# Performance work log

Measured on AMD Instinct MI355X. Metric: run time of the kernel, lower is better.

## Reference

```python
import jax, jax.numpy as jnp
import numpy as np

# ---- model dims (match init_kwargs) ----
B, L, D_MODEL = 2, 4096, 1024
EXPAND = 2
D_INNER = EXPAND * D_MODEL          # 2048
D_STATE = 128
D_CONV = 4
HEADDIM = 64
NHEADS = D_INNER // HEADDIM         # 32
NGROUPS = 1
CHUNK = 256
CONV_DIM = D_INNER + 2 * NGROUPS * D_STATE   # 2304
D_IN = 2 * D_INNER + 2 * NGROUPS * D_STATE + NHEADS  # 4384
EPS = 1e-5
DT_MIN, DT_MAX, DT_FLOOR = 0.001, 0.1, 1e-4
DT_LIMIT = (0.0, 100.0)
CONV_INIT = 0.5


def setup_inputs() -> dict:
    key = jax.random.key(0)
    ks = jax.random.split(key, 6)
    zxbcdt = jax.random.normal(ks[0], (B, L, D_IN), jnp.float32)
    conv_weight = jax.random.uniform(ks[1], (CONV_DIM, D_CONV), jnp.float32, -CONV_INIT, CONV_INIT)
    conv_b = jax.random.normal(ks[2], (CONV_DIM,), jnp.float32) * 0.01
    # dt_bias init: inverse softplus of dt sampled log-uniform in [dt_min, dt_max]
    dt = jnp.exp(jax.random.uniform(ks[3], (NHEADS,), jnp.float32) * (np.log(DT_MAX) - np.log(DT_MIN)) + np.log(DT_MIN))
    dt = jnp.clip(dt, DT_FLOOR, None)
    dt_bias = dt + jnp.log(-jnp.expm1(-dt))
    A_log = jnp.log(jax.random.uniform(ks[4], (NHEADS,), jnp.float32, 1.0, 16.0))
    Dparam = jnp.ones((NHEADS,), jnp.float32)
    norm_weight = jnp.ones((D_INNER,), jnp.float32)
    return dict(zxbcdt=zxbcdt, conv_weight=conv_weight, conv_b=conv_b,
                dt_bias=dt_bias, A_log=A_log, Dparam=Dparam, norm_weight=norm_weight)


def _segsum(x):
    """x: (..., T) -> (..., T, T), entry [i,j] = sum_{j<k<=i} x[k], -inf above diag."""
    T = x.shape[-1]
    xc = jnp.cumsum(x, axis=-1)
    seg = xc[..., :, None] - xc[..., None, :]
    mask = jnp.tril(jnp.ones((T, T), dtype=bool))
    return jnp.where(mask, seg, -jnp.inf)


def _ssd(x, a, Bm, Cm, chunk):
    """Chunked SSD (Mamba2). x:(b,l,h,p) already dt-scaled, a:(b,l,h)=dt*A,
    Bm/Cm:(b,l,h,n). Returns y:(b,l,h,p)."""
    b, l, h, p = x.shape
    n = Bm.shape[-1]
    c = l // chunk
    x = x.reshape(b, c, chunk, h, p)
    Bm = Bm.reshape(b, c, chunk, h, n)
    Cm = Cm.reshape(b, c, chunk, h, n)
    a = a.reshape(b, c, chunk, h).transpose(0, 3, 1, 2)  # (b,h,c,cl)
    a_cs = jnp.cumsum(a, axis=-1)                        # (b,h,c,cl)
    # 1) intra-chunk (diagonal blocks)
    Lmat = jnp.exp(_segsum(a))                           # (b,h,c,cl,cl)
    Y_diag = jnp.einsum('bclhn,bcshn,bhcls,bcshp->bclhp', Cm, Bm, Lmat, x)
    # 2) chunk final states
    decay_states = jnp.exp(a_cs[..., -1:] - a_cs)        # (b,h,c,cl)
    states = jnp.einsum('bclhn,bhcl,bclhp->bchpn', Bm, decay_states, x)
    states = jnp.concatenate([jnp.zeros_like(states[:, :1]), states], axis=1)  # (b,c+1,h,p,n)
    # 3) inter-chunk recurrence
    chunk_sum = jnp.pad(a_cs[..., -1], ((0, 0), (0, 0), (1, 0)))  # (b,h,c+1)
    decay_chunk = jnp.exp(_segsum(chunk_sum))            # (b,h,c+1,c+1)
    new_states = jnp.einsum('bhzc,bchpn->bzhpn', decay_chunk, states)
    prev_states = new_states[:, :-1]                     # (b,c,h,p,n)
    # 4) state -> output contribution
    Y_off = jnp.einsum('bclhn,bchpn,bhcl->bclhp', Cm, prev_states, jnp.exp(a_cs))
    return (Y_diag + Y_off).reshape(b, l, h, p)


def reference(zxbcdt, conv_weight, conv_b, dt_bias, A_log, Dparam, norm_weight):
    z, xBC, dt_raw = jnp.split(zxbcdt, [D_INNER, D_INNER + CONV_DIM], axis=-1)
    # depthwise causal conv1d (padding=d_conv-1, truncate to L) + SiLU
    xp = jnp.pad(xBC, ((0, 0), (D_CONV - 1, 0), (0, 0)))
    conv = conv_b
    for k in range(D_CONV):  # small fixed kernel width
        conv = conv + conv_weight[:, k] * xp[:, k:k + L, :]
    xBC = jax.nn.silu(conv)
    x, Bm, Cm = jnp.split(xBC, [D_INNER, D_INNER + NGROUPS * D_STATE], axis=-1)
    x = x.reshape(B, L, NHEADS, HEADDIM)
    hpg = NHEADS // NGROUPS
    Bm = jnp.repeat(Bm.reshape(B, L, NGROUPS, D_STATE), hpg, axis=2)  # (B,L,H,N)
    Cm = jnp.repeat(Cm.reshape(B, L, NGROUPS, D_STATE), hpg, axis=2)
    dt = jax.nn.softplus(dt_raw + dt_bias)               # (B,L,H)
    dt = jnp.clip(dt, DT_LIMIT[0], DT_LIMIT[1])
    A = -jnp.exp(A_log)                                  # (H,)
    y = _ssd(x * dt[..., None], dt * A, Bm, Cm, CHUNK)   # (B,L,H,P)
    y = y + x * Dparam[None, None, :, None]              # skip term D*x
    y = y.reshape(B, L, D_INNER)
    # gated RMSNorm (norm_before_gate=False): normalize(y * silu(z)) * w
    y = y * jax.nn.silu(z)
    y = y * jax.lax.rsqrt(jnp.mean(y * y, axis=-1, keepdims=True) + EPS) * norm_weight
    return y
```

## Files before the change

### kernel.cpp

```cpp
#include <hip/hip_runtime.h>
#include <hip/hip_bf16.h>

#define NB 2
#define LSEQ 4096
#define DIN 4384
#define DINNER 2048
#define DSTATE 128
#define CONVD 2304
#define HD 64
#define NH 32
#define CK 256
#define NCH 16

typedef __attribute__((ext_vector_type(8))) short bfrag;
typedef __attribute__((ext_vector_type(4))) float ffrag;

__device__ __forceinline__ float bf2f(unsigned short u){ return __uint_as_float(((unsigned int)u)<<16); }
__device__ __forceinline__ unsigned short f2bf(float f){
  unsigned int u = __float_as_uint(f);
  unsigned int r = (u + 0x7fffu + ((u>>16)&1u)) >> 16;
  return (unsigned short)r;
}
__device__ __forceinline__ unsigned int pk2(float a, float b){
  return (unsigned)f2bf(a) | ((unsigned)f2bf(b) << 16);
}
__device__ __forceinline__ float blo(unsigned int u){ return __uint_as_float(u<<16); }
__device__ __forceinline__ float bhi(unsigned int u){ return __uint_as_float(u & 0xffff0000u); }
__device__ __forceinline__ bfrag pack8(const float* f){
  bfrag r;
  #pragma unroll
  for (int i=0;i<8;i++) r[i] = (short)f2bf(f[i]);
  return r;
}

__global__ __launch_bounds__(256) void k_conv(const float* __restrict__ zx,
    const float* __restrict__ cw, const float* __restrict__ cb,
    unsigned short* __restrict__ xconv)
{
  int bid = blockIdx.x;
  int ct = bid % 9;
  int rt = bid / 9;
  int b = rt >> 6, lt = rt & 63;
  int t = threadIdx.x;
  int q = t & 63, lg = t >> 6;
  int c0 = ct*256 + q*4;
  const float* colp = zx + (size_t)b*LSEQ*DIN + DINNER + c0;
  float4 w0 = *(const float4*)&cw[(c0+0)*4];
  float4 w1 = *(const float4*)&cw[(c0+1)*4];
  float4 w2 = *(const float4*)&cw[(c0+2)*4];
  float4 w3 = *(const float4*)&cw[(c0+3)*4];
  float4 bias = *(const float4*)&cb[c0];
  int l0 = lt*64 + lg*16;
  float4 win0, win1, win2, win3;
  win0 = (l0-3 >= 0) ? *(const float4*)(colp + (size_t)(l0-3)*DIN) : make_float4(0,0,0,0);
  win1 = (l0-2 >= 0) ? *(const float4*)(colp + (size_t)(l0-2)*DIN) : make_float4(0,0,0,0);
  win2 = (l0-1 >= 0) ? *(const float4*)(colp + (size_t)(l0-1)*DIN) : make_float4(0,0,0,0);
  unsigned short* op = xconv + (size_t)(b*LSEQ)*CONVD + c0;
  #pragma unroll 4
  for (int i=0;i<16;i++){
    int l = l0 + i;
    win3 = *(const float4*)(colp + (size_t)l*DIN);
    float o0 = bias.x + w0.x*win0.x + w0.y*win1.x + w0.z*win2.x + w0.w*win3.x;
    float o1 = bias.y + w1.x*win0.y + w1.y*win1.y + w1.z*win2.y + w1.w*win3.y;
    float o2 = bias.z + w2.x*win0.z + w2.y*win1.z + w2.z*win2.z + w2.w*win3.z;
    float o3 = bias.w + w3.x*win0.w + w3.y*win1.w + w3.z*win2.w + w3.w*win3.w;
    o0 = o0 / (1.f + __expf(-o0));
    o1 = o1 / (1.f + __expf(-o1));
    o2 = o2 / (1.f + __expf(-o2));
    o3 = o3 / (1.f + __expf(-o3));
    uint2 pk; pk.x = pk2(o0,o1); pk.y = pk2(o2,o3);
    *(uint2*)&op[(size_t)l*CONVD] = pk;
    win0 = win1; win1 = win2; win2 = win3;
  }
}

__global__ __launch_bounds__(256) void k_dt(const float* __restrict__ zx,
    const float* __restrict__ dtb, float* __restrict__ dtv)
{
  int idx = blockIdx.x*256 + threadIdx.x;
  int l = idx & (LSEQ-1);
  int bh = idx >> 12;
  int h = bh & 31, b = bh >> 5;
  float x = zx[(size_t)(b*LSEQ + l)*DIN + DINNER + CONVD + h] + dtb[h];
  float sp = (x > 20.f) ? x : log1pf(__expf(x));
  dtv[idx] = fminf(sp, 100.f);
}

__global__ __launch_bounds__(256) void k_tr(const unsigned short* __restrict__ xconv,
    unsigned short* __restrict__ btg)
{
  __shared__ unsigned short sT[128][72];
  int bid = blockIdx.x;
  int b = bid >> 6, tile = bid & 63;
  int l0 = tile * 64;
  int t = threadIdx.x;
  #pragma unroll
  for (int k=0;k<32;k++){
    int idx = 256*k + t;
    int l = idx >> 7, n = idx & 127;
    sT[n][l] = xconv[(size_t)(b*LSEQ + l0 + l)*CONVD + DINNER + n];
  }
  __syncthreads();
  #pragma unroll
  for (int k=0;k<32;k++){
    int idx = 256*k + t;
    int n = idx >> 6, l = idx & 63;
    btg[(size_t)(b*DSTATE + n)*LSEQ + l0 + l] = sT[n][l];
  }
}

__constant__ int g_lt[10] = {0,1,1,2,2,2,3,3,3,3};
__constant__ int g_st[10] = {0,0,1,0,1,2,0,1,2,3};
__global__ __launch_bounds__(256) void k_gmat(const unsigned short* __restrict__ xconv,
    unsigned short* __restrict__ G)
{
  int bid = blockIdx.x;
  int pr = bid % 10;
  int cc = bid / 10;
  int c = cc & 15, b = cc >> 4;
  int lt = g_lt[pr], st = g_st[pr];
  int t = threadIdx.x, lane = t & 63, wv = t >> 6;
  int cq = lane & 15, g = lane >> 4;
  const unsigned short* base = xconv + (size_t)(b*LSEQ + c*CK)*CONVD;
  ffrag acc[4];
  #pragma unroll
  for (int ss=0; ss<4; ++ss){ acc[ss][0]=0.f; acc[ss][1]=0.f; acc[ss][2]=0.f; acc[ss][3]=0.f; }
  #pragma unroll
  for (int ks=0; ks<4; ++ks){
    int nb = 32*ks + 8*g;
    int l = lt*64 + 16*wv + cq;
    bfrag afr = *(const bfrag*)(base + (size_t)l*CONVD + DINNER + DSTATE + nb);
    #pragma unroll
    for (int ss=0; ss<4; ++ss){
      int s = st*64 + 16*ss + cq;
      bfrag bfr = *(const bfrag*)(base + (size_t)s*CONVD + DINNER + nb);
      acc[ss] = __builtin_amdgcn_mfma_f32_16x16x32_bf16(afr, bfr, acc[ss], 0,0,0);
    }
  }
  unsigned short* gp = G + (size_t)(b*NCH + c)*CK*CK;
  #pragma unroll
  for (int ss=0; ss<4; ++ss)
    #pragma unroll
    for (int j=0; j<4; ++j){
      int l = lt*64 + 16*wv + 4*g + j, s = st*64 + 16*ss + cq;
      gp[(size_t)l*CK + s] = f2bf(acc[ss][j]);
    }
}

__global__ __launch_bounds__(256) void k_states(const unsigned short* __restrict__ xconv,
   const unsigned short* __restrict__ btg,
   const float* __restrict__ dtv, const float* __restrict__ alog,
   unsigned short* __restrict__ states,
   float* __restrict__ acsg2)
{
  int bid = blockIdx.x;
  int h = bid & 31, c = (bid>>5)&15, b = bid>>9;
  int t = threadIdx.x, lane = t & 63, wv = t >> 6;
  int cq = lane & 15, g = lane >> 4;
  __shared__ float s_acs2[CK];
  __shared__ float s_w[CK];
  __shared__ float s_dt[CK];
  __shared__ unsigned short s_xsT[64][256];

  const float LOG2E = 1.44269504088896340736f;
  float dtl = dtv[(size_t)(b*NH + h)*LSEQ + c*CK + t];
  float a2 = dtl * (-__expf(alog[h])) * LOG2E;
  s_dt[t] = dtl;
  s_acs2[t] = a2;
  __syncthreads();
  #pragma unroll
  for (int off=1; off<256; off<<=1){
    float v = (t>=off) ? s_acs2[t-off] : 0.f;
    __syncthreads();
    s_acs2[t] += v;
    __syncthreads();
  }
  float a2last = s_acs2[CK-1];
  s_w[t] = exp2f(a2last - s_acs2[t]);
  acsg2[((size_t)(b*NCH + c)*NH + h)*CK + t] = s_acs2[t];
  {
    const unsigned short* xp = xconv + (size_t)(b*LSEQ + c*CK)*CONVD + h*HD;
    int p = t & 63;
    int lw = t >> 6;
    #pragma unroll 8
    for (int k=0;k<64;k++){
      int l = 4*k + lw;
      float x = bf2f(xp[(size_t)l*CONVD + p]);
      s_xsT[p][l ^ ((p&7)<<3)] = f2bf(x * s_dt[l]);
    }
  }
  __syncthreads();

  ffrag acc[4][2];
  #pragma unroll
  for (int ps=0;ps<4;ps++)
    #pragma unroll
    for (int ns=0;ns<2;ns++){ acc[ps][ns][0]=0.f; acc[ps][ns][1]=0.f; acc[ps][ns][2]=0.f; acc[ps][ns][3]=0.f; }
  const unsigned short* btp = btg + (size_t)b*DSTATE*LSEQ + c*CK;
  #pragma unroll 2
  for (int ks=0; ks<8; ++ks){
    int lb = 32*ks + 8*g;
    float4 w0 = *(const float4*)&s_w[lb];
    float4 w1 = *(const float4*)&s_w[lb+4];
    bfrag bfr[2];
    #pragma unroll
    for (int ns=0; ns<2; ++ns){
      int n = 32*wv + 16*ns + cq;
      bfr[ns] = *(const bfrag*)(btp + (size_t)n*LSEQ + lb);
    }
    bfrag afr[4];
    #pragma unroll
    for (int ps=0; ps<4; ++ps){
      int p = 16*ps + cq;
      bfrag xv = *(const bfrag*)&s_xsT[p][lb ^ ((p&7)<<3)];
      float f[8];
      f[0]=bf2f((unsigned short)xv[0])*w0.x; f[1]=bf2f((unsigned short)xv[1])*w0.y;
      f[2]=bf2f((unsigned short)xv[2])*w0.z; f[3]=bf2f((unsigned short)xv[3])*w0.w;
      f[4]=bf2f((unsigned short)xv[4])*w1.x; f[5]=bf2f((unsigned short)xv[5])*w1.y;
      f[6]=bf2f((unsigned short)xv[6])*w1.z; f[7]=bf2f((unsigned short)xv[7])*w1.w;
      afr[ps] = pack8(f);
    }
    #pragma unroll
    for (int ps=0; ps<4; ++ps)
      #pragma unroll
      for (int ns=0; ns<2; ++ns)
        acc[ps][ns] = __builtin_amdgcn_mfma_f32_16x16x32_bf16(afr[ps], bfr[ns], acc[ps][ns], 0,0,0);
  }
  size_t sbase = ((size_t)((b*NCH + c)*NH + h))*HD*DSTATE;
  #pragma unroll
  for (int ps=0; ps<4; ++ps)
    #pragma unroll
    for (int ns=0; ns<2; ++ns)
      #pragma unroll
      for (int j=0; j<4; ++j){
        int p = 16*ps + 4*g + j, n = 32*wv + 16*ns + cq;
        states[sbase + (size_t)p*DSTATE + n] = f2bf(acc[ps][ns][j]);
      }
}

__global__ __launch_bounds__(256) void k_scan(unsigned short* __restrict__ states,
    const float* __restrict__ acsg2)
{
  int bid = blockIdx.x;
  int sub = bid & 7, h = (bid>>3) & 31, b = bid >> 8;
  int t = threadIdx.x;
  int e0 = sub*1024 + t*4;
  float c0=0.f, c1=0.f, c2=0.f, c3=0.f;
  for (int c=0;c<NCH;c++){
    float dec = exp2f(acsg2[((size_t)(b*NCH + c)*NH + h)*CK + (CK-1)]);
    size_t base = ((size_t)((b*NCH + c)*NH + h))*HD*DSTATE + e0;
    uint2 v = *(uint2*)&states[base];
    float u0 = blo(v.x), u1 = bhi(v.x), u2 = blo(v.y), u3 = bhi(v.y);
    uint2 w; w.x = pk2(c0,c1); w.y = pk2(c2,c3);
    *(uint2*)&states[base] = w;
    c0 = dec*c0 + u0; c1 = dec*c1 + u1; c2 = dec*c2 + u2; c3 = dec*c3 + u3;
  }
}

__global__ __launch_bounds__(256) void k_Y(const unsigned short* __restrict__ xconv,
   const float* __restrict__ dtv,
   const unsigned short* __restrict__ G,
   const unsigned short* __restrict__ states,
   const float* __restrict__ acsg2,
   unsigned short* __restrict__ ybuf)
{
  int bid = blockIdx.x;
  int h = bid & 31, c = (bid>>5)&15, b = bid>>9;
  int t = threadIdx.x, lane = t & 63, wv = t >> 6;
  int cq = lane & 15, g = lane >> 4;
  __shared__ float s_acs2[CK];
  __shared__ float s_dt[CK];
  __shared__ unsigned short s_xsT[64][256];

  s_acs2[t] = acsg2[((size_t)(b*NCH + c)*NH + h)*CK + t];
  s_dt[t] = dtv[(size_t)(b*NH + h)*LSEQ + c*CK + t];
  __syncthreads();
  {
    const unsigned short* xp = xconv + (size_t)(b*LSEQ + c*CK)*CONVD + h*HD;
    int p = t & 63;
    int lw = t >> 6;
    #pragma unroll 8
    for (int k=0;k<64;k++){
      int l = 4*k + lw;
      float x = bf2f(xp[(size_t)l*CONVD + p]);
      s_xsT[p][l ^ ((p&7)<<3)] = f2bf(x * s_dt[l]);
    }
  }
  __syncthreads();

  ffrag acc[4][4];
  #pragma unroll
  for (int ls=0;ls<4;ls++)
    #pragma unroll
    for (int ps=0;ps<4;ps++){ acc[ls][ps][0]=0.f; acc[ls][ps][1]=0.f; acc[ls][ps][2]=0.f; acc[ls][ps][3]=0.f; }
  float a2l[4];
  #pragma unroll
  for (int ls=0; ls<4; ++ls) a2l[ls] = s_acs2[64*wv + 16*ls + cq];

  const unsigned short* gp = G + (size_t)(b*NCH + c)*CK*CK;
  int nks = 2*wv + 2;
  for (int ks=0; ks<nks; ++ks){
    int sb = 32*ks + 8*g;
    float4 e0 = *(const float4*)&s_acs2[sb];
    float4 e1 = *(const float4*)&s_acs2[sb+4];
    float a2s[8] = {e0.x,e0.y,e0.z,e0.w,e1.x,e1.y,e1.z,e1.w};
    bfrag bfr[4];
    #pragma unroll
    for (int ps=0; ps<4; ++ps){
      int p = 16*ps + cq;
      bfr[ps] = *(const bfrag*)&s_xsT[p][sb ^ ((p&7)<<3)];
    }
    bfrag afr[4];
    #pragma unroll
    for (int ls=0; ls<4; ++ls){
      int l = 64*wv + 16*ls + cq;
      bfrag gv = *(const bfrag*)(gp + (size_t)l*CK + sb);
      float f[8];
      #pragma unroll
      for (int i=0;i<8;i++){
        int s = sb + i;
        float cf = exp2f(a2l[ls] - a2s[i]);
        cf = (s <= l) ? cf : 0.f;
        f[i] = bf2f((unsigned short)gv[i]) * cf;
      }
      afr[ls] = pack8(f);
    }
    #pragma unroll
    for (int ls=0; ls<4; ++ls)
      #pragma unroll
      for (int ps=0; ps<4; ++ps)
        acc[ls][ps] = __builtin_amdgcn_mfma_f32_16x16x32_bf16(afr[ls], bfr[ps], acc[ls][ps], 0,0,0);
  }

  {
    float el[4];
    #pragma unroll
    for (int ls=0; ls<4; ++ls) el[ls] = exp2f(a2l[ls]);
    const unsigned short* crow = xconv + (size_t)(b*LSEQ + c*CK)*CONVD + DINNER + DSTATE;
    const unsigned short* psb = states + ((size_t)((b*NCH + c)*NH + h))*HD*DSTATE;
    #pragma unroll
    for (int ks=0; ks<4; ++ks){
      int nb = 32*ks + 8*g;
      bfrag bfr[4];
      #pragma unroll
      for (int pp=0; pp<4; ++pp)
        bfr[pp] = *(const bfrag*)(psb + (size_t)(16*pp + cq)*DSTATE + nb);
      bfrag afr[4];
      #pragma unroll
      for (int ls=0; ls<4; ++ls){
        int l = 64*wv + 16*ls + cq;
        bfrag cv = *(const bfrag*)(crow + (size_t)l*CONVD + nb);
        float f[8];
        #pragma unroll
        for (int i=0;i<8;i++) f[i] = bf2f((unsigned short)cv[i]) * el[ls];
        afr[ls] = pack8(f);
      }
      #pragma unroll
      for (int ls=0; ls<4; ++ls)
        #pragma unroll
        for (int pp=0; pp<4; ++pp)
          acc[ls][pp] = __builtin_amdgcn_mfma_f32_16x16x32_bf16(afr[ls], bfr[pp], acc[ls][pp], 0,0,0);
    }
  }

  unsigned short* yrow = ybuf + (size_t)(b*LSEQ + c*CK)*DINNER + h*HD;
  #pragma unroll
  for (int ls=0; ls<4; ++ls)
    #pragma unroll
    for (int ps=0; ps<4; ++ps)
      #pragma unroll
      for (int j=0; j<4; ++j){
        int l = 64*wv + 16*ls + 4*g + j, p = 16*ps + cq;
        yrow[(size_t)l*DINNER + p] = f2bf(acc[ls][ps][j]);
      }
}

__global__ __launch_bounds__(256) void k_final(const float* __restrict__ zx,
  const unsigned short* __restrict__ xconv, const unsigned short* __restrict__ ybuf,
  const float* __restrict__ dpar, const float* __restrict__ nw,
  float* __restrict__ out)
{
  int row = blockIdx.x;
  int t = threadIdx.x;
  int d0 = 8*t;
  const float* zrow = zx + (size_t)row*DIN;
  const unsigned short* xrow = xconv + (size_t)row*CONVD;
  const unsigned short* yrow = ybuf + (size_t)row*DINNER;
  float vals[8];
  float ss = 0.f;
  uint4 yv = *(const uint4*)&yrow[d0];
  uint4 xv = *(const uint4*)&xrow[d0];
  float4 z0 = *(const float4*)&zrow[d0];
  float4 z1 = *(const float4*)&zrow[d0+4];
  float dp = dpar[d0 >> 6];
  float yf[8], xf[8];
  yf[0]=blo(yv.x); yf[1]=bhi(yv.x); yf[2]=blo(yv.y); yf[3]=bhi(yv.y);
  yf[4]=blo(yv.z); yf[5]=bhi(yv.z); yf[6]=blo(yv.w); yf[7]=bhi(yv.w);
  xf[0]=blo(xv.x); xf[1]=bhi(xv.x); xf[2]=blo(xv.y); xf[3]=bhi(xv.y);
  xf[4]=blo(xv.z); xf[5]=bhi(xv.z); xf[6]=blo(xv.w); xf[7]=bhi(xv.w);
  float zf[8] = {z0.x,z0.y,z0.z,z0.w,z1.x,z1.y,z1.z,z1.w};
  #pragma unroll
  for (int e=0;e<8;e++){
    float y = yf[e] + xf[e]*dp;
    float z = zf[e];
    y *= z / (1.f + __expf(-z));
    vals[e] = y;
    ss += y*y;
  }
  #pragma unroll
  for (int off=1; off<64; off<<=1) ss += __shfl_xor(ss, off, 64);
  __shared__ float red[4];
  if ((t & 63) == 0) red[t>>6] = ss;
  __syncthreads();
  float tot = red[0]+red[1]+red[2]+red[3];
  float rms = rsqrtf(tot * (1.f/(float)DINNER) + 1e-5f);
  float* orow = out + (size_t)row*DINNER;
  float4 w0 = *(const float4*)&nw[d0];
  float4 w1 = *(const float4*)&nw[d0+4];
  float4 o0, o1;
  o0.x = vals[0]*rms*w0.x; o0.y = vals[1]*rms*w0.y;
  o0.z = vals[2]*rms*w0.z; o0.w = vals[3]*rms*w0.w;
  o1.x = vals[4]*rms*w1.x; o1.y = vals[5]*rms*w1.y;
  o1.z = vals[6]*rms*w1.z; o1.w = vals[7]*rms*w1.w;
  *(float4*)&orow[d0] = o0;
  *(float4*)&orow[d0+4] = o1;
}

extern "C" void kernel_launch(void* const* d_in, const int* in_sizes, int n_in,
                              void* d_out, int out_size, void* d_ws, size_t ws_size,
                              hipStream_t stream)
{
  const float* zx   = (const float*)d_in[0];
  const float* cw   = (const float*)d_in[1];
  const float* cb   = (const float*)d_in[2];
  const float* dtb  = (const float*)d_in[3];
  const float* alog = (const float*)d_in[4];
  const float* dpar = (const float*)d_in[5];
  const float* nw   = (const float*)d_in[6];
  float* out = (float*)d_out;
  char* ws = (char*)d_ws;

  unsigned short* xconv  = (unsigned short*)(ws);
  unsigned short* btg    = (unsigned short*)(ws + 37748736);
  float*          dtv    = (float*)(ws + 39845888);
  float*          acsg2  = (float*)(ws + 40894464);
  unsigned short* states = (unsigned short*)(ws + 41943040);
  unsigned short* G      = (unsigned short*)(ws + 58720256);
  unsigned short* ybuf   = (unsigned short*)(ws + 62914560);

  hipLaunchKernelGGL(k_conv,   dim3(NB*64*9), dim3(256), 0, stream, zx, cw, cb, xconv);
  hipLaunchKernelGGL(k_dt,     dim3(1024),  dim3(256), 0, stream, zx, dtb, dtv);
  hipLaunchKernelGGL(k_tr,     dim3(NB*64), dim3(256), 0, stream, xconv, btg);
  hipLaunchKernelGGL(k_gmat,   dim3(NB*NCH*10), dim3(256), 0, stream, xconv, G);
  hipLaunchKernelGGL(k_states, dim3(NB*NCH*NH), dim3(256), 0, stream, xconv, btg, dtv, alog, states, acsg2);
  hipLaunchKernelGGL(k_scan,   dim3(NB*NH*8),  dim3(256), 0, stream, states, acsg2);
  hipLaunchKernelGGL(k_Y,      dim3(NB*NCH*NH), dim3(256), 0, stream, xconv, dtv, G, states, acsg2, ybuf);
  hipLaunchKernelGGL(k_final,  dim3(NB*LSEQ), dim3(256), 0, stream, zx, xconv, ybuf, dpar, nw, out);
}
```

Measured before the change: 342.9 us.

## Merge small kernels, use hardware bf16 pack, wave-shuffle scan, precompute weights

Merges the dt, B-transpose and G-matrix kernels into one launch, split by block-index ranges. Replaces software bf16 rounding with the v_cvt_pk_bf16_f32 instruction and the shared-memory scan in k_states with a wave shuffle scan. It also folds the decay weight into the staged x tile so the MFMA loop needs no per-element rescaling. In k_Y, the inter-chunk C·state term now runs first with a post-scale by exp(acs), and intra-chunk decay factors come from a running product instead of one exp2 per element, which changes rounding slightly.

```diff
diff --git a/kernel.cpp b/kernel.cpp
--- a/kernel.cpp
+++ b/kernel.cpp
@@ -26,11 +26,16 @@
 }
 __device__ __forceinline__ float blo(unsigned int u){ return __uint_as_float(u<<16); }
 __device__ __forceinline__ float bhi(unsigned int u){ return __uint_as_float(u & 0xffff0000u); }
-__device__ __forceinline__ bfrag pack8(const float* f){
-  bfrag r;
-  #pragma unroll
-  for (int i=0;i<8;i++) r[i] = (short)f2bf(f[i]);
+__device__ __forceinline__ unsigned int cvtpk(float a, float b){
+  unsigned int r;
+  asm("v_cvt_pk_bf16_f32 %0, %1, %2" : "=v"(r) : "v"(a), "v"(b));
   return r;
+}
+__device__ __forceinline__ bfrag pack8c(const float* f){
+  union { unsigned int u[4]; bfrag b; } r;
+  r.u[0]=cvtpk(f[0],f[1]); r.u[1]=cvtpk(f[2],f[3]);
+  r.u[2]=cvtpk(f[4],f[5]); r.u[3]=cvtpk(f[6],f[7]);
+  return r.b;
 }
 
 __global__ __launch_bounds__(256) void k_conv(const float* __restrict__ zx,
@@ -68,83 +73,80 @@
     o1 = o1 / (1.f + __expf(-o1));
     o2 = o2 / (1.f + __expf(-o2));
     o3 = o3 / (1.f + __expf(-o3));
-    uint2 pk; pk.x = pk2(o0,o1); pk.y = pk2(o2,o3);
+    uint2 pk; pk.x = cvtpk(o0,o1); pk.y = cvtpk(o2,o3);
     *(uint2*)&op[(size_t)l*CONVD] = pk;
     win0 = win1; win1 = win2; win2 = win3;
   }
 }
 
-__global__ __launch_bounds__(256) void k_dt(const float* __restrict__ zx,
-    const float* __restrict__ dtb, float* __restrict__ dtv)
-{
-  int idx = blockIdx.x*256 + threadIdx.x;
-  int l = idx & (LSEQ-1);
-  int bh = idx >> 12;
-  int h = bh & 31, b = bh >> 5;
-  float x = zx[(size_t)(b*LSEQ + l)*DIN + DINNER + CONVD + h] + dtb[h];
-  float sp = (x > 20.f) ? x : log1pf(__expf(x));
-  dtv[idx] = fminf(sp, 100.f);
-}
-
-__global__ __launch_bounds__(256) void k_tr(const unsigned short* __restrict__ xconv,
-    unsigned short* __restrict__ btg)
+__constant__ int g_lt[10] = {0,1,1,2,2,2,3,3,3,3};
+__constant__ int g_st[10] = {0,0,1,0,1,2,0,1,2,3};
+__global__ __launch_bounds__(256) void k_misc(const float* __restrict__ zx,
+    const float* __restrict__ dtb,
+    const unsigned short* __restrict__ xconv,
+    float* __restrict__ dtv, unsigned short* __restrict__ btg,
+    unsigned short* __restrict__ G)
 {
   __shared__ unsigned short sT[128][72];
   int bid = blockIdx.x;
-  int b = bid >> 6, tile = bid & 63;
-  int l0 = tile * 64;
   int t = threadIdx.x;
-  #pragma unroll
-  for (int k=0;k<32;k++){
-    int idx = 256*k + t;
-    int l = idx >> 7, n = idx & 127;
-    sT[n][l] = xconv[(size_t)(b*LSEQ + l0 + l)*CONVD + DINNER + n];
-  }
-  __syncthreads();
-  #pragma unroll
-  for (int k=0;k<32;k++){
-    int idx = 256*k + t;
-    int n = idx >> 6, l = idx & 63;
-    btg[(size_t)(b*DSTATE + n)*LSEQ + l0 + l] = sT[n][l];
-  }
-}
-
-__constant__ int g_lt[10] = {0,1,1,2,2,2,3,3,3,3};
-__constant__ int g_st[10] = {0,0,1,0,1,2,0,1,2,3};
-__global__ __launch_bounds__(256) void k_gmat(const unsigned short* __restrict__ xconv,
-    unsigned short* __restrict__ G)
-{
-  int bid = blockIdx.x;
-  int pr = bid % 10;
-  int cc = bid / 10;
-  int c = cc & 15, b = cc >> 4;
-  int lt = g_lt[pr], st = g_st[pr];
-  int t = threadIdx.x, lane = t & 63, wv = t >> 6;
-  int cq = lane & 15, g = lane >> 4;
-  const unsigned short* base = xconv + (size_t)(b*LSEQ + c*CK)*CONVD;
-  ffrag acc[4];
-  #pragma unroll
-  for (int ss=0; ss<4; ++ss){ acc[ss][0]=0.f; acc[ss][1]=0.f; acc[ss][2]=0.f; acc[ss][3]=0.f; }
-  #pragma unroll
-  for (int ks=0; ks<4; ++ks){
-    int nb = 32*ks + 8*g;
-    int l = lt*64 + 16*wv + cq;
-    bfrag afr = *(const bfrag*)(base + (size_t)l*CONVD + DINNER + DSTATE + nb);
-    #pragma unroll
-    for (int ss=0; ss<4; ++ss){
-      int s = st*64 + 16*ss + cq;
-      bfrag bfr = *(const bfrag*)(base + (size_t)s*CONVD + DINNER + nb);
-      acc[ss] = __builtin_amdgcn_mfma_f32_16x16x32_bf16(afr, bfr, acc[ss], 0,0,0);
-    }
-  }
-  unsigned short* gp = G + (size_t)(b*NCH + c)*CK*CK;
-  #pragma unroll
-  for (int ss=0; ss<4; ++ss)
-    #pragma unroll
-    for (int j=0; j<4; ++j){
-      int l = lt*64 + 16*wv + 4*g + j, s = st*64 + 16*ss + cq;
-      gp[(size_t)l*CK + s] = f2bf(acc[ss][j]);
-    }
+  if (bid < 320){
+    int pr = bid % 10;
+    int cc = bid / 10;
+    int c = cc & 15, b = cc >> 4;
+    int lt = g_lt[pr], st = g_st[pr];
+    int lane = t & 63, wv = t >> 6;
+    int cq = lane & 15, g = lane >> 4;
+    const unsigned short* base = xconv + (size_t)(b*LSEQ + c*CK)*CONVD;
+    ffrag acc[4];
+    #pragma unroll
+    for (int ss=0; ss<4; ++ss){ acc[ss][0]=0.f; acc[ss][1]=0.f; acc[ss][2]=0.f; acc[ss][3]=0.f; }
+    #pragma unroll
+    for (int ks=0; ks<4; ++ks){
+      int nb = 32*ks + 8*g;
+      int l = lt*64 + 16*wv + cq;
+      bfrag afr = *(const bfrag*)(base + (size_t)l*CONVD + DINNER + DSTATE + nb);
+      #pragma unroll
+      for (int ss=0; ss<4; ++ss){
+        int s = st*64 + 16*ss + cq;
+        bfrag bfr = *(const bfrag*)(base + (size_t)s*CONVD + DINNER + nb);
+        acc[ss] = __builtin_amdgcn_mfma_f32_16x16x32_bf16(afr, bfr, acc[ss], 0,0,0);
+      }
+    }
+    unsigned short* gp = G + (size_t)(b*NCH + c)*CK*CK;
+    #pragma unroll
+    for (int ss=0; ss<4; ++ss)
+      #pragma unroll
+      for (int j=0; j<4; ++j){
+        int l = lt*64 + 16*wv + 4*g + j, s = st*64 + 16*ss + cq;
+        gp[(size_t)l*CK + s] = f2bf(acc[ss][j]);
+      }
+  } else if (bid < 448){
+    int bid2 = bid - 320;
+    int b = bid2 >> 6, tile = bid2 & 63;
+    int l0 = tile * 64;
+    #pragma unroll
+    for (int k=0;k<32;k++){
+      int idx = 256*k + t;
+      int l = idx >> 7, n = idx & 127;
+      sT[n][l] = xconv[(size_t)(b*LSEQ + l0 + l)*CONVD + DINNER + n];
+    }
+    __syncthreads();
+    #pragma unroll
+    for (int k=0;k<32;k++){
+      int idx = 256*k + t;
+      int n = idx >> 6, l = idx & 63;
+      btg[(size_t)(b*DSTATE + n)*LSEQ + l0 + l] = sT[n][l];
+    }
+  } else {
+    int idx = (bid-448)*256 + t;
+    int l = idx & (LSEQ-1);
+    int bh = idx >> 12;
+    int h = bh & 31, b = bh >> 5;
+    float x = zx[(size_t)(b*LSEQ + l)*DIN + DINNER + CONVD + h] + dtb[h];
+    float sp = (x > 20.f) ? x : log1pf(__expf(x));
+    dtv[idx] = fminf(sp, 100.f);
+  }
 }
 
 __global__ __launch_bounds__(256) void k_states(const unsigned short* __restrict__ xconv,
@@ -157,36 +159,39 @@
   int h = bid & 31, c = (bid>>5)&15, b = bid>>9;
   int t = threadIdx.x, lane = t & 63, wv = t >> 6;
   int cq = lane & 15, g = lane >> 4;
-  __shared__ float s_acs2[CK];
   __shared__ float s_w[CK];
-  __shared__ float s_dt[CK];
+  __shared__ float s_wt[4];
   __shared__ unsigned short s_xsT[64][256];
 
   const float LOG2E = 1.44269504088896340736f;
   float dtl = dtv[(size_t)(b*NH + h)*LSEQ + c*CK + t];
   float a2 = dtl * (-__expf(alog[h])) * LOG2E;
-  s_dt[t] = dtl;
-  s_acs2[t] = a2;
-  __syncthreads();
-  #pragma unroll
-  for (int off=1; off<256; off<<=1){
-    float v = (t>=off) ? s_acs2[t-off] : 0.f;
-    __syncthreads();
-    s_acs2[t] += v;
-    __syncthreads();
-  }
-  float a2last = s_acs2[CK-1];
-  s_w[t] = exp2f(a2last - s_acs2[t]);
-  acsg2[((size_t)(b*NCH + c)*NH + h)*CK + t] = s_acs2[t];
+  float sc = a2;
+  #pragma unroll
+  for (int off=1; off<64; off<<=1){
+    float v = __shfl_up(sc, off, 64);
+    if (lane >= off) sc += v;
+  }
+  if (lane == 63) s_wt[wv] = sc;
+  __syncthreads();
+  float offacc = 0.f;
+  #pragma unroll
+  for (int w2=0; w2<4; ++w2) offacc += (w2 < wv) ? s_wt[w2] : 0.f;
+  float acs = sc + offacc;
+  float tot = s_wt[0]+s_wt[1]+s_wt[2]+s_wt[3];
+  s_w[t] = dtl * exp2f(tot - acs);
+  acsg2[((size_t)(b*NCH + c)*NH + h)*CK + t] = acs;
+  __syncthreads();
   {
     const unsigned short* xp = xconv + (size_t)(b*LSEQ + c*CK)*CONVD + h*HD;
-    int p = t & 63;
-    int lw = t >> 6;
+    int p = t & 63, lw = t >> 6;
+    int sw = (p&7)<<3;
     #pragma unroll 8
-    for (int k=0;k<64;k++){
-      int l = 4*k + lw;
-      float x = bf2f(xp[(size_t)l*CONVD + p]);
-      s_xsT[p][l ^ ((p&7)<<3)] = f2bf(x * s_dt[l]);
+    for (int k=0;k<32;k++){
+      int l = 8*k + 2*lw;
+      float x0 = bf2f(xp[(size_t)l*CONVD + p]) * s_w[l];
+      float x1 = bf2f(xp[(size_t)(l+1)*CONVD + p]) * s_w[l+1];
+      *(unsigned int*)&s_xsT[p][l ^ sw] = cvtpk(x0, x1);
     }
   }
   __syncthreads();
@@ -200,31 +205,20 @@
   #pragma unroll 2
   for (int ks=0; ks<8; ++ks){
     int lb = 32*ks + 8*g;
-    float4 w0 = *(const float4*)&s_w[lb];
-    float4 w1 = *(const float4*)&s_w[lb+4];
     bfrag bfr[2];
     #pragma unroll
     for (int ns=0; ns<2; ++ns){
       int n = 32*wv + 16*ns + cq;
       bfr[ns] = *(const bfrag*)(btp + (size_t)n*LSEQ + lb);
     }
-    bfrag afr[4];
     #pragma unroll
     for (int ps=0; ps<4; ++ps){
       int p = 16*ps + cq;
-      bfrag xv = *(const bfrag*)&s_xsT[p][lb ^ ((p&7)<<3)];
-      float f[8];
-      f[0]=bf2f((unsigned short)xv[0])*w0.x; f[1]=bf2f((unsigned short)xv[1])*w0.y;
-      f[2]=bf2f((unsigned short)xv[2])*w0.z; f[3]=bf2f((unsigned short)xv[3])*w0.w;
-      f[4]=bf2f((unsigned short)xv[4])*w1.x; f[5]=bf2f((unsigned short)xv[5])*w1.y;
-      f[6]=bf2f((unsigned short)xv[6])*w1.z; f[7]=bf2f((unsigned short)xv[7])*w1.w;
-      afr[ps] = pack8(f);
-    }
-    #pragma unroll
-    for (int ps=0; ps<4; ++ps)
+      bfrag afr = *(const bfrag*)&s_xsT[p][lb ^ ((p&7)<<3)];
       #pragma unroll
       for (int ns=0; ns<2; ++ns)
-        acc[ps][ns] = __builtin_amdgcn_mfma_f32_16x16x32_bf16(afr[ps], bfr[ns], acc[ps][ns], 0,0,0);
+        acc[ps][ns] = __builtin_amdgcn_mfma_f32_16x16x32_bf16(afr, bfr[ns], acc[ps][ns], 0,0,0);
+    }
   }
   size_t sbase = ((size_t)((b*NCH + c)*NH + h))*HD*DSTATE;
   #pragma unroll
@@ -251,7 +245,7 @@
     size_t base = ((size_t)((b*NCH + c)*NH + h))*HD*DSTATE + e0;
     uint2 v = *(uint2*)&states[base];
     float u0 = blo(v.x), u1 = bhi(v.x), u2 = blo(v.y), u3 = bhi(v.y);
-    uint2 w; w.x = pk2(c0,c1); w.y = pk2(c2,c3);
+    uint2 w; w.x = cvtpk(c0,c1); w.y = cvtpk(c2,c3);
     *(uint2*)&states[base] = w;
     c0 = dec*c0 + u0; c1 = dec*c1 + u1; c2 = dec*c2 + u2; c3 = dec*c3 + u3;
   }
@@ -277,13 +271,14 @@
   __syncthreads();
   {
     const unsigned short* xp = xconv + (size_t)(b*LSEQ + c*CK)*CONVD + h*HD;
-    int p = t & 63;
-    int lw = t >> 6;
+    int p = t & 63, lw = t >> 6;
+    int sw = (p&7)<<3;
     #pragma unroll 8
-    for (int k=0;k<64;k++){
-      int l = 4*k + lw;
-      float x = bf2f(xp[(size_t)l*CONVD + p]);
-      s_xsT[p][l ^ ((p&7)<<3)] = f2bf(x * s_dt[l]);
+    for (int k=0;k<32;k++){
+      int l = 8*k + 2*lw;
+      float x0 = bf2f(xp[(size_t)l*CONVD + p]) * s_dt[l];
+      float x1 = bf2f(xp[(size_t)(l+1)*CONVD + p]) * s_dt[l+1];
+      *(unsigned int*)&s_xsT[p][l ^ sw] = cvtpk(x0, x1);
     }
   }
   __syncthreads();
@@ -293,10 +288,39 @@
   for (int ls=0;ls<4;ls++)
     #pragma unroll
     for (int ps=0;ps<4;ps++){ acc[ls][ps][0]=0.f; acc[ls][ps][1]=0.f; acc[ls][ps][2]=0.f; acc[ls][ps][3]=0.f; }
+
+  {
+    const unsigned short* crow = xconv + (size_t)(b*LSEQ + c*CK)*CONVD + DINNER + DSTATE;
+    const unsigned short* psb = states + ((size_t)((b*NCH + c)*NH + h))*HD*DSTATE;
+    #pragma unroll
+    for (int ks=0; ks<4; ++ks){
+      int nb = 32*ks + 8*g;
+      bfrag bfr[4];
+      #pragma unroll
+      for (int pp=0; pp<4; ++pp)
+        bfr[pp] = *(const bfrag*)(psb + (size_t)(16*pp + cq)*DSTATE + nb);
+      #pragma unroll
+      for (int ls=0; ls<4; ++ls){
+        int l = 64*wv + 16*ls + cq;
+        bfrag afr = *(const bfrag*)(crow + (size_t)l*CONVD + nb);
+        #pragma unroll
+        for (int pp=0; pp<4; ++pp)
+          acc[ls][pp] = __builtin_amdgcn_mfma_f32_16x16x32_bf16(afr, bfr[pp], acc[ls][pp], 0,0,0);
+      }
+    }
+    #pragma unroll
+    for (int ls=0; ls<4; ++ls)
+      #pragma unroll
+      for (int j=0; j<4; ++j){
+        float el = exp2f(s_acs2[64*wv + 16*ls + 4*g + j]);
+        #pragma unroll
+        for (int ps=0; ps<4; ++ps) acc[ls][ps][j] *= el;
+      }
+  }
+
   float a2l[4];
   #pragma unroll
   for (int ls=0; ls<4; ++ls) a2l[ls] = s_acs2[64*wv + 16*ls + cq];
-
   const unsigned short* gp = G + (size_t)(b*NCH + c)*CK*CK;
   int nks = 2*wv + 2;
   for (int ks=0; ks<nks; ++ks){
@@ -304,63 +328,38 @@
     float4 e0 = *(const float4*)&s_acs2[sb];
     float4 e1 = *(const float4*)&s_acs2[sb+4];
     float a2s[8] = {e0.x,e0.y,e0.z,e0.w,e1.x,e1.y,e1.z,e1.w};
-    bfrag bfr[4];
+    float ddn[8];
+    #pragma unroll
+    for (int i=1;i<8;i++) ddn[i] = exp2f(a2s[i] - a2s[i-1]);
+    bfrag bfrx[4];
     #pragma unroll
     for (int ps=0; ps<4; ++ps){
       int p = 16*ps + cq;
-      bfr[ps] = *(const bfrag*)&s_xsT[p][sb ^ ((p&7)<<3)];
+      bfrx[ps] = *(const bfrag*)&s_xsT[p][sb ^ ((p&7)<<3)];
     }
     bfrag afr[4];
     #pragma unroll
     for (int ls=0; ls<4; ++ls){
       int l = 64*wv + 16*ls + cq;
+      int di = l - sb;
+      int astar = (di < 7) ? di : 7;
+      float aval = exp2f(a2l[ls] - s_acs2[sb + astar]);
       bfrag gv = *(const bfrag*)(gp + (size_t)l*CK + sb);
-      float f[8];
-      #pragma unroll
-      for (int i=0;i<8;i++){
-        int s = sb + i;
-        float cf = exp2f(a2l[ls] - a2s[i]);
-        cf = (s <= l) ? cf : 0.f;
-        f[i] = bf2f((unsigned short)gv[i]) * cf;
-      }
-      afr[ls] = pack8(f);
+      float run = 0.f;
+      float ff[8];
+      #pragma unroll
+      for (int i=7;i>=0;--i){
+        run = (i == astar) ? aval : run;
+        ff[i] = bf2f((unsigned short)gv[i]) * run;
+        if (i) run *= ddn[i];
+      }
+      afr[ls] = pack8c(ff);
     }
     #pragma unroll
     for (int ls=0; ls<4; ++ls)
       #pragma unroll
       for (int ps=0; ps<4; ++ps)
-        acc[ls][ps] = __builtin_amdgcn_mfma_f32_16x16x32_bf16(afr[ls], bfr[ps], acc[ls][ps], 0,0,0);
-  }
-
-  {
-    float el[4];
-    #pragma unroll
-    for (int ls=0; ls<4; ++ls) el[ls] = exp2f(a2l[ls]);
-    const unsigned short* crow = xconv + (size_t)(b*LSEQ + c*CK)*CONVD + DINNER + DSTATE;
-    const unsigned short* psb = states + ((size_t)((b*NCH + c)*NH + h))*HD*DSTATE;
-    #pragma unroll
-    for (int ks=0; ks<4; ++ks){
-      int nb = 32*ks + 8*g;
-      bfrag bfr[4];
-      #pragma unroll
-      for (int pp=0; pp<4; ++pp)
-        bfr[pp] = *(const bfrag*)(psb + (size_t)(16*pp + cq)*DSTATE + nb);
-      bfrag afr[4];
-      #pragma unroll
-      for (int ls=0; ls<4; ++ls){
-        int l = 64*wv + 16*ls + cq;
-        bfrag cv = *(const bfrag*)(crow + (size_t)l*CONVD + nb);
-        float f[8];
-        #pragma unroll
-        for (int i=0;i<8;i++) f[i] = bf2f((unsigned short)cv[i]) * el[ls];
-        afr[ls] = pack8(f);
-      }
-      #pragma unroll
-      for (int ls=0; ls<4; ++ls)
-        #pragma unroll
-        for (int pp=0; pp<4; ++pp)
-          acc[ls][pp] = __builtin_amdgcn_mfma_f32_16x16x32_bf16(afr[ls], bfr[pp], acc[ls][pp], 0,0,0);
-    }
+        acc[ls][ps] = __builtin_amdgcn_mfma_f32_16x16x32_bf16(afr[ls], bfrx[ps], acc[ls][ps], 0,0,0);
   }
 
   unsigned short* yrow = ybuf + (size_t)(b*LSEQ + c*CK)*DINNER + h*HD;
@@ -449,9 +448,7 @@
   unsigned short* ybuf   = (unsigned short*)(ws + 62914560);
 
   hipLaunchKernelGGL(k_conv,   dim3(NB*64*9), dim3(256), 0, stream, zx, cw, cb, xconv);
-  hipLaunchKernelGGL(k_dt,     dim3(1024),  dim3(256), 0, stream, zx, dtb, dtv);
-  hipLaunchKernelGGL(k_tr,     dim3(NB*64), dim3(256), 0, stream, xconv, btg);
-  hipLaunchKernelGGL(k_gmat,   dim3(NB*NCH*10), dim3(256), 0, stream, xconv, G);
+  hipLaunchKernelGGL(k_misc,   dim3(1472), dim3(256), 0, stream, zx, dtb, xconv, dtv, btg, G);
   hipLaunchKernelGGL(k_states, dim3(NB*NCH*NH), dim3(256), 0, stream, xconv, btg, dtv, alog, states, acsg2);
   hipLaunchKernelGGL(k_scan,   dim3(NB*NH*8),  dim3(256), 0, stream, states, acsg2);
   hipLaunchKernelGGL(k_Y,      dim3(NB*NCH*NH), dim3(256), 0, stream, xconv, dtv, G, states, acsg2, ybuf);
```

Result: faster. 327.2 us (-4.6%).
